# Performance work log

Hardware: AMD Instinct MI355X
Metric: run time of the kernel (lower is better)

Reference implementation:

```python
import jax, jax.numpy as jnp
import numpy as np

TOP_K = 2

def setup_inputs() -> dict:
    key = jax.random.key(0)
    k0, k1, k2, k3 = jax.random.split(key, 4)
    B, S, H, I, E = 2, 2048, 1024, 1408, 8
    hidden_states = jax.random.normal(k0, (B, S, H), dtype=jnp.float32)
    router_weight = jax.random.normal(k1, (E, H), dtype=jnp.float32) * 0.02
    gate_up_proj = jax.random.normal(k2, (E, 2 * I, H), dtype=jnp.float32) * 0.02
    down_proj = jax.random.normal(k3, (E, H, I), dtype=jnp.float32) * 0.02
    return {
        "hidden_states": hidden_states,
        "router_weight": router_weight,
        "gate_up_proj": gate_up_proj,
        "down_proj": down_proj,
    }

def reference(hidden_states, router_weight, gate_up_proj, down_proj):
    B, S, H = hidden_states.shape
    E = router_weight.shape[0]
    x = hidden_states.reshape(-1, H)                       # [T, H]
    T = x.shape[0]
    # Router: logits -> float32 softmax -> top-k (matches torch: topk on probs)
    logits = x @ router_weight.T                           # [T, E]
    probs = jax.nn.softmax(logits.astype(jnp.float32), axis=-1)
    topw, topi = jax.lax.top_k(probs, TOP_K)               # [T, K]
    topw = topw.astype(x.dtype)
    # Per-token combine weights over experts (zero for non-selected experts).
    combine = jnp.zeros((T, E), dtype=x.dtype)
    combine = combine.at[jnp.arange(T)[:, None], topi].set(topw)  # [T, E]
    # Dense grouped expert compute (same math as gather-GEMM-scatter loop:
    # tokens not routed to expert e get combine weight 0).
    gu = jnp.einsum('th,eoh->teo', x, gate_up_proj)        # [T, E, 2I]
    g, u = jnp.split(gu, 2, axis=-1)                       # [T, E, I] each
    h = jax.nn.silu(g) * u                                 # [T, E, I]
    y = jnp.einsum('tei,ehi->teh', h, down_proj)           # [T, E, H]
    out = jnp.einsum('teh,te->th', y, combine)             # [T, H]
    return out.reshape(B, S, H)
```

## Files before the change

kernel.cpp:

```cpp
#include <hip/hip_runtime.h>
#include <math.h>

#define NTOK 4096
#define HDIM 1024
#define NEXP 8
#define IDIM 1408
#define TWO_I 2816
#define BM 128
#define BK 32
#define NRB 72
#define ROWCAP (NRB * BM)

typedef _Float16 f16x8 __attribute__((ext_vector_type(8)));
typedef float f32x4 __attribute__((ext_vector_type(4)));

typedef __attribute__((address_space(1))) const unsigned int gu32;
typedef __attribute__((address_space(3))) unsigned int lu32;
__device__ __forceinline__ void async16(const void* g, void* l) {
  __builtin_amdgcn_global_load_lds((gu32*)g, (lu32*)l, 16, 0, 0);
}

__device__ __forceinline__ void seg_prefix(const int* __restrict__ counts, int* aof) {
  int o = 0; aof[0] = 0;
#pragma unroll
  for (int i = 0; i < 8; i++) { o += (counts[i] + 127) & ~127; aof[i + 1] = o; }
}

extern "C" __global__ void moe_init(int* counts, int* cursor, int* tok) {
  int i = blockIdx.x * 256 + threadIdx.x;
  if (i < NEXP) { counts[i] = 0; cursor[i] = 0; }
  if (i < ROWCAP) tok[i] = -1;
}

#define NG8 (NEXP * TWO_I * HDIM / 8)
#define ND8 (NEXP * HDIM * IDIM / 8)
extern "C" __global__ void moe_cvtw(const float* __restrict__ gup, const float* __restrict__ dp,
                                    _Float16* __restrict__ guph, _Float16* __restrict__ dph) {
  int i = blockIdx.x * 256 + threadIdx.x;
  const float4* s; uint4* d; size_t idx;
  if (i < NG8) { s = (const float4*)gup; d = (uint4*)guph; idx = i; }
  else if (i < NG8 + ND8) { s = (const float4*)dp; d = (uint4*)dph; idx = i - NG8; }
  else return;
  float4 a = s[idx * 2], b = s[idx * 2 + 1];
  union { _Float16 h[8]; uint4 u; } p;
  p.h[0] = (_Float16)a.x; p.h[1] = (_Float16)a.y; p.h[2] = (_Float16)a.z; p.h[3] = (_Float16)a.w;
  p.h[4] = (_Float16)b.x; p.h[5] = (_Float16)b.y; p.h[6] = (_Float16)b.z; p.h[7] = (_Float16)b.w;
  d[idx] = p.u;
}

extern "C" __global__ void moe_router(const float* __restrict__ x,
                                      const float* __restrict__ rw,
                                      int* __restrict__ topi,
                                      float* __restrict__ topw,
                                      _Float16* __restrict__ xh) {
  int w = threadIdx.x >> 6, lane = threadIdx.x & 63;
  int t = blockIdx.x * 4 + w;
  const float4* xp = (const float4*)(x + (size_t)t * HDIM);
  const float4* rp = (const float4*)rw;
  float acc[NEXP];
#pragma unroll
  for (int e = 0; e < NEXP; e++) acc[e] = 0.f;
#pragma unroll
  for (int i = 0; i < HDIM / 256; i++) {
    float4 xv = xp[i * 64 + lane];
    union { _Float16 h[4]; uint2 u; } pk;
    pk.h[0] = (_Float16)xv.x; pk.h[1] = (_Float16)xv.y;
    pk.h[2] = (_Float16)xv.z; pk.h[3] = (_Float16)xv.w;
    *(uint2*)(xh + (size_t)t * HDIM + i * 256 + lane * 4) = pk.u;
#pragma unroll
    for (int e = 0; e < NEXP; e++) {
      float4 rv = rp[e * 256 + i * 64 + lane];
      acc[e] += xv.x * rv.x + xv.y * rv.y + xv.z * rv.z + xv.w * rv.w;
    }
  }
#pragma unroll
  for (int e = 0; e < NEXP; e++) {
#pragma unroll
    for (int off = 32; off > 0; off >>= 1) acc[e] += __shfl_down(acc[e], off);
  }
  if (lane == 0) {
    float m = acc[0];
    for (int e = 1; e < NEXP; e++) m = fmaxf(m, acc[e]);
    float p[NEXP], s = 0.f;
    for (int e = 0; e < NEXP; e++) { p[e] = __expf(acc[e] - m); s += p[e]; }
    float inv = 1.f / s;
    int i0 = 0; float b0 = p[0];
    for (int e = 1; e < NEXP; e++) if (p[e] > b0) { b0 = p[e]; i0 = e; }
    int i1 = -1; float b1 = -1.f;
    for (int e = 0; e < NEXP; e++) if (e != i0 && p[e] > b1) { b1 = p[e]; i1 = e; }
    topi[t * 2] = i0; topi[t * 2 + 1] = i1;
    topw[t * 2] = b0 * inv; topw[t * 2 + 1] = b1 * inv;
  }
}

extern "C" __global__ void moe_count(const int* __restrict__ topi, int* __restrict__ counts) {
  __shared__ int cnt[NEXP];
  if (threadIdx.x < NEXP) cnt[threadIdx.x] = 0;
  __syncthreads();
  int t = blockIdx.x * 256 + threadIdx.x;
  atomicAdd(&cnt[topi[t * 2]], 1);
  atomicAdd(&cnt[topi[t * 2 + 1]], 1);
  __syncthreads();
  if (threadIdx.x < NEXP) atomicAdd(&counts[threadIdx.x], cnt[threadIdx.x]);
}

extern "C" __global__ void moe_scatter(const int* __restrict__ topi, const float* __restrict__ topw,
                                       const int* __restrict__ counts, int* __restrict__ cursor,
                                       int* __restrict__ tok, float* __restrict__ wrow,
                                       int* __restrict__ rows) {
  __shared__ int cnt[NEXP];
  __shared__ int base[NEXP];
  int aof[9]; seg_prefix(counts, aof);
  int tid = threadIdx.x;
  if (tid < NEXP) cnt[tid] = 0;
  __syncthreads();
  int t = blockIdx.x * 256 + tid;
  int e0 = topi[t * 2], e1 = topi[t * 2 + 1];
  int r0 = atomicAdd(&cnt[e0], 1);
  int r1 = atomicAdd(&cnt[e1], 1);
  __syncthreads();
  if (tid < NEXP) base[tid] = atomicAdd(&cursor[tid], cnt[tid]);
  __syncthreads();
  int row0 = aof[e0] + base[e0] + r0;
  int row1 = aof[e1] + base[e1] + r1;
  tok[row0] = t; wrow[row0] = topw[t * 2];     rows[t * 2]     = row0;
  tok[row1] = t; wrow[row1] = topw[t * 2 + 1]; rows[t * 2 + 1] = row1;
}

union SM1 {
  struct { _Float16 a[BM * BK]; _Float16 b[BM * BK]; } st;
  _Float16 ubuf[BM * 66];
};

extern "C" __global__ __launch_bounds__(256) void moe_gemm1(
    const _Float16* __restrict__ xh, const _Float16* __restrict__ guph,
    const int* __restrict__ counts, const int* __restrict__ tok,
    _Float16* __restrict__ hbuf) {
  __shared__ __align__(16) SM1 sm;
  int aof[9]; seg_prefix(counts, aof);
  int fid = blockIdx.x;
  int g = fid & 7, t7 = fid >> 3;
  int jl = t7 % 11, u = t7 / 11;
  int r = u % 9, jh = u / 9;
  int j = jh * 11 + jl;
  int rb = g + 8 * r;
  int row0 = rb * BM;
  if (row0 >= aof[8]) return;
  int e = 0;
#pragma unroll
  for (int i = 0; i < 8; i++) if (row0 >= aof[i]) e = i;

  const int tid = threadIdx.x;
  const int lane = tid & 63, w = tid >> 6;
  const int wm = w & 1, wn = w >> 1;
  const int quad = lane >> 4, l15 = lane & 15;

  f32x4 acc[4][4];
#pragma unroll
  for (int im = 0; im < 4; im++)
#pragma unroll
    for (int in = 0; in < 4; in++) acc[im][in] = (f32x4){0.f, 0.f, 0.f, 0.f};

  const int lq = lane >> 2;
  const int ls = lane & 3;
  const int gsl = ls ^ ((lq >> 1) & 3);
  const int rA0 = w * 16 + lq, rA1 = rA0 + 64;
  int tA0 = tok[row0 + rA0]; tA0 = tA0 < 0 ? 0 : tA0;
  int tA1 = tok[row0 + rA1]; tA1 = tA1 < 0 ? 0 : tA1;
  const _Float16* gA0 = xh + (size_t)tA0 * HDIM + gsl * 8;
  const _Float16* gA1 = xh + (size_t)tA1 * HDIM + gsl * 8;
  const _Float16* eb = guph + (size_t)e * TWO_I * HDIM;
  const _Float16* gB0 = eb + (size_t)(j * 64 + rA0) * HDIM + gsl * 8;
  const _Float16* gB1 = eb + (size_t)(IDIM + j * 64 + rA0) * HDIM + gsl * 8;
  _Float16* lA0 = &sm.st.a[w * 512];
  _Float16* lA1 = &sm.st.a[(w + 4) * 512];
  _Float16* lB0 = &sm.st.b[w * 512];
  _Float16* lB1 = &sm.st.b[(w + 4) * 512];

  const int qsw = (quad ^ ((l15 >> 1) & 3)) * 8;

  for (int kb = 0; kb < HDIM / BK; kb++) {
    async16(gA0, lA0); async16(gA1, lA1);
    async16(gB0, lB0); async16(gB1, lB1);
    gA0 += BK; gA1 += BK; gB0 += BK; gB1 += BK;
    __syncthreads();
    f16x8 av[4], bv[4];
#pragma unroll
    for (int im = 0; im < 4; im++)
      av[im] = *(const f16x8*)&sm.st.a[(wm * 64 + im * 16 + l15) * BK + qsw];
#pragma unroll
    for (int in = 0; in < 4; in++)
      bv[in] = *(const f16x8*)&sm.st.b[(wn * 64 + in * 16 + l15) * BK + qsw];
#pragma unroll
    for (int im = 0; im < 4; im++)
#pragma unroll
      for (int in = 0; in < 4; in++)
        acc[im][in] = __builtin_amdgcn_mfma_f32_16x16x32_f16(av[im], bv[in], acc[im][in], 0, 0, 0);
    __syncthreads();
  }

  if (wn == 1) {
#pragma unroll
    for (int im = 0; im < 4; im++)
#pragma unroll
      for (int in = 0; in < 4; in++)
#pragma unroll
        for (int r2 = 0; r2 < 4; r2++)
          sm.ubuf[(wm * 64 + im * 16 + quad * 4 + r2) * 66 + in * 16 + l15] = (_Float16)acc[im][in][r2];
  }
  __syncthreads();
  if (wn == 0) {
#pragma unroll
    for (int im = 0; im < 4; im++)
#pragma unroll
      for (int in = 0; in < 4; in++)
#pragma unroll
        for (int r2 = 0; r2 < 4; r2++) {
          float gg = acc[im][in][r2];
          float uu = (float)sm.ubuf[(wm * 64 + im * 16 + quad * 4 + r2) * 66 + in * 16 + l15];
          float hh = gg / (1.f + __expf(-gg)) * uu;
          int row = row0 + wm * 64 + im * 16 + quad * 4 + r2;
          hbuf[(size_t)row * IDIM + j * 64 + in * 16 + l15] = (_Float16)hh;
        }
  }
}

extern "C" __global__ __launch_bounds__(256) void moe_gemm2(
    const _Float16* __restrict__ hbuf, const _Float16* __restrict__ dph,
    const int* __restrict__ counts, const float* __restrict__ wrow,
    _Float16* __restrict__ yh) {
  __shared__ __align__(16) struct { _Float16 a[BM * BK]; _Float16 b[BM * BK]; } sm;
  int aof[9]; seg_prefix(counts, aof);
  int fid = blockIdx.x;
  int g = fid & 7, t7 = fid >> 3;
  int cb = t7 & 7, r = t7 >> 3;
  int rb = g + 8 * r;
  int row0 = rb * BM;
  if (row0 >= aof[8]) return;
  int e = 0;
#pragma unroll
  for (int i = 0; i < 8; i++) if (row0 >= aof[i]) e = i;

  const int tid = threadIdx.x;
  const int lane = tid & 63, w = tid >> 6;
  const int wm = w & 1, wn = w >> 1;
  const int quad = lane >> 4, l15 = lane & 15;

  f32x4 acc[4][4];
#pragma unroll
  for (int im = 0; im < 4; im++)
#pragma unroll
    for (int in = 0; in < 4; in++) acc[im][in] = (f32x4){0.f, 0.f, 0.f, 0.f};

  const int lq = lane >> 2, ls = lane & 3;
  const int gsl = ls ^ ((lq >> 1) & 3);
  const int rA0 = w * 16 + lq;
  const _Float16* gA0 = hbuf + (size_t)(row0 + rA0) * IDIM + gsl * 8;
  const _Float16* gA1 = gA0 + (size_t)64 * IDIM;
  const _Float16* eb = dph + (size_t)e * HDIM * IDIM;
  const _Float16* gB0 = eb + (size_t)(cb * 128 + rA0) * IDIM + gsl * 8;
  const _Float16* gB1 = gB0 + (size_t)64 * IDIM;
  _Float16* lA0 = &sm.a[w * 512];
  _Float16* lA1 = &sm.a[(w + 4) * 512];
  _Float16* lB0 = &sm.b[w * 512];
  _Float16* lB1 = &sm.b[(w + 4) * 512];

  const int qsw = (quad ^ ((l15 >> 1) & 3)) * 8;

  for (int kb = 0; kb < IDIM / BK; kb++) {
    async16(gA0, lA0); async16(gA1, lA1);
    async16(gB0, lB0); async16(gB1, lB1);
    gA0 += BK; gA1 += BK; gB0 += BK; gB1 += BK;
    __syncthreads();
    f16x8 av[4], bv[4];
#pragma unroll
    for (int im = 0; im < 4; im++)
      av[im] = *(const f16x8*)&sm.a[(wm * 64 + im * 16 + l15) * BK + qsw];
#pragma unroll
    for (int in = 0; in < 4; in++)
      bv[in] = *(const f16x8*)&sm.b[(wn * 64 + in * 16 + l15) * BK + qsw];
#pragma unroll
    for (int im = 0; im < 4; im++)
#pragma unroll
      for (int in = 0; in < 4; in++)
        acc[im][in] = __builtin_amdgcn_mfma_f32_16x16x32_f16(av[im], bv[in], acc[im][in], 0, 0, 0);
    __syncthreads();
  }

#pragma unroll
  for (int im = 0; im < 4; im++) {
#pragma unroll
    for (int r2 = 0; r2 < 4; r2++) {
      int row = row0 + wm * 64 + im * 16 + quad * 4 + r2;
      float wgt = wrow[row];
#pragma unroll
      for (int in = 0; in < 4; in++) {
        int col = cb * 128 + wn * 64 + in * 16 + l15;
        yh[(size_t)row * HDIM + col] = (_Float16)(acc[im][in][r2] * wgt);
      }
    }
  }
}

extern "C" __global__ void moe_combine(const _Float16* __restrict__ yh,
                                       const int* __restrict__ rows,
                                       float* __restrict__ out) {
  int i = blockIdx.x * 256 + threadIdx.x;
  int t = i >> 7, c8 = i & 127;
  int rA = rows[t * 2], rB = rows[t * 2 + 1];
  union { uint4 u; _Float16 h[8]; } pa, pb;
  pa.u = ((const uint4*)(yh + (size_t)rA * HDIM))[c8];
  pb.u = ((const uint4*)(yh + (size_t)rB * HDIM))[c8];
  float4 o0, o1;
  o0.x = (float)pa.h[0] + (float)pb.h[0]; o0.y = (float)pa.h[1] + (float)pb.h[1];
  o0.z = (float)pa.h[2] + (float)pb.h[2]; o0.w = (float)pa.h[3] + (float)pb.h[3];
  o1.x = (float)pa.h[4] + (float)pb.h[4]; o1.y = (float)pa.h[5] + (float)pb.h[5];
  o1.z = (float)pa.h[6] + (float)pb.h[6]; o1.w = (float)pa.h[7] + (float)pb.h[7];
  ((float4*)out)[(size_t)i * 2] = o0;
  ((float4*)out)[(size_t)i * 2 + 1] = o1;
}

extern "C" void kernel_launch(void* const* d_in, const int* in_sizes, int n_in,
                              void* d_out, int out_size, void* d_ws, size_t ws_size,
                              hipStream_t stream) {
  const float* x   = (const float*)d_in[0];
  const float* rw  = (const float*)d_in[1];
  const float* gup = (const float*)d_in[2];
  const float* dp  = (const float*)d_in[3];
  float* out = (float*)d_out;

  char* ws = (char*)d_ws;
  int*   counts = (int*)ws;
  int*   cursor = (int*)(ws + 64);
  int*   topi   = (int*)(ws + 4096);
  float* topw   = (float*)(ws + 36864);
  int*   tok    = (int*)(ws + 69632);
  float* wrow   = (float*)(ws + 106496);
  int*   rows   = (int*)(ws + 143360);
  _Float16* xh   = (_Float16*)(ws + 176128);
  _Float16* guph = (_Float16*)(ws + 8564736);
  _Float16* dph  = (_Float16*)(ws + 54702080);
  _Float16* hbuf = (_Float16*)(ws + 77770752);
  _Float16* yh   = (_Float16*)(ws + 103723008);

  moe_init<<<(ROWCAP + 255) / 256, 256, 0, stream>>>(counts, cursor, tok);
  moe_router<<<NTOK / 4, 256, 0, stream>>>(x, rw, topi, topw, xh);
  moe_count<<<NTOK / 256, 256, 0, stream>>>(topi, counts);
  moe_scatter<<<NTOK / 256, 256, 0, stream>>>(topi, topw, counts, cursor, tok, wrow, rows);
  moe_cvtw<<<(NG8 + ND8 + 255) / 256, 256, 0, stream>>>(gup, dp, guph, dph);
  moe_gemm1<<<8 * 22 * 9, 256, 0, stream>>>(xh, guph, counts, tok, hbuf);
  moe_gemm2<<<8 * 8 * 9, 256, 0, stream>>>(hbuf, dph, counts, wrow, yh);
  moe_combine<<<NTOK * HDIM / 8 / 256, 256, 0, stream>>>(yh, rows, out);
}
```

Measured before the change: 339.2 us.

## Double K-tile per barrier and remap row blocks contiguously per XCD group

Both GEMM kernels now load a 64-wide K slab as two 32-wide LDS halves per iteration, which halves the number of barrier pairs and keeps more loads in flight. The block-to-row-block mapping is also reworked so that each of the 8 block groups (fid & 7) gets a contiguous range of real row blocks sized from the actual row count. Empty blocks exit early instead of striding past the end, which aims to balance work and improve L2 locality of expert weights. LDS use doubles, which could reduce occupancy. The remap also relies on the grid launching enough blocks per group.

```diff
diff --git a/kernel.cpp b/kernel.cpp
--- a/kernel.cpp
+++ b/kernel.cpp
@@ -7,7 +7,6 @@
 #define IDIM 1408
 #define TWO_I 2816
 #define BM 128
-#define BK 32
 #define NRB 72
 #define ROWCAP (NRB * BM)
 
@@ -128,7 +127,7 @@
 }
 
 union SM1 {
-  struct { _Float16 a[BM * BK]; _Float16 b[BM * BK]; } st;
+  struct { _Float16 a[2][BM * 32]; _Float16 b[2][BM * 32]; } st;
   _Float16 ubuf[BM * 66];
 };
 
@@ -138,14 +137,16 @@
     _Float16* __restrict__ hbuf) {
   __shared__ __align__(16) SM1 sm;
   int aof[9]; seg_prefix(counts, aof);
+  int nl = aof[8] >> 7;
   int fid = blockIdx.x;
-  int g = fid & 7, t7 = fid >> 3;
-  int jl = t7 % 11, u = t7 / 11;
-  int r = u % 9, jh = u / 9;
+  int g = fid & 7, s = fid >> 3;
+  int rb0 = (g * nl) >> 3, ng = (((g + 1) * nl) >> 3) - rb0;
+  if (s >= ng * 22) return;
+  int jl = s % 11, u = s / 11;
+  int r = u % ng, jh = u / ng;
   int j = jh * 11 + jl;
-  int rb = g + 8 * r;
+  int rb = rb0 + r;
   int row0 = rb * BM;
-  if (row0 >= aof[8]) return;
   int e = 0;
 #pragma unroll
   for (int i = 0; i < 8; i++) if (row0 >= aof[i]) e = i;
@@ -172,30 +173,35 @@
   const _Float16* eb = guph + (size_t)e * TWO_I * HDIM;
   const _Float16* gB0 = eb + (size_t)(j * 64 + rA0) * HDIM + gsl * 8;
   const _Float16* gB1 = eb + (size_t)(IDIM + j * 64 + rA0) * HDIM + gsl * 8;
-  _Float16* lA0 = &sm.st.a[w * 512];
-  _Float16* lA1 = &sm.st.a[(w + 4) * 512];
-  _Float16* lB0 = &sm.st.b[w * 512];
-  _Float16* lB1 = &sm.st.b[(w + 4) * 512];
+  _Float16* lA0k0 = &sm.st.a[0][w * 512];        _Float16* lA0k1 = &sm.st.a[1][w * 512];
+  _Float16* lA1k0 = &sm.st.a[0][(w + 4) * 512];  _Float16* lA1k1 = &sm.st.a[1][(w + 4) * 512];
+  _Float16* lB0k0 = &sm.st.b[0][w * 512];        _Float16* lB0k1 = &sm.st.b[1][w * 512];
+  _Float16* lB1k0 = &sm.st.b[0][(w + 4) * 512];  _Float16* lB1k1 = &sm.st.b[1][(w + 4) * 512];
 
   const int qsw = (quad ^ ((l15 >> 1) & 3)) * 8;
 
-  for (int kb = 0; kb < HDIM / BK; kb++) {
-    async16(gA0, lA0); async16(gA1, lA1);
-    async16(gB0, lB0); async16(gB1, lB1);
-    gA0 += BK; gA1 += BK; gB0 += BK; gB1 += BK;
+  for (int kb = 0; kb < HDIM / 64; kb++) {
+    async16(gA0, lA0k0); async16(gA0 + 32, lA0k1);
+    async16(gA1, lA1k0); async16(gA1 + 32, lA1k1);
+    async16(gB0, lB0k0); async16(gB0 + 32, lB0k1);
+    async16(gB1, lB1k0); async16(gB1 + 32, lB1k1);
+    gA0 += 64; gA1 += 64; gB0 += 64; gB1 += 64;
     __syncthreads();
-    f16x8 av[4], bv[4];
-#pragma unroll
-    for (int im = 0; im < 4; im++)
-      av[im] = *(const f16x8*)&sm.st.a[(wm * 64 + im * 16 + l15) * BK + qsw];
-#pragma unroll
-    for (int in = 0; in < 4; in++)
-      bv[in] = *(const f16x8*)&sm.st.b[(wn * 64 + in * 16 + l15) * BK + qsw];
-#pragma unroll
-    for (int im = 0; im < 4; im++)
+#pragma unroll
+    for (int kh = 0; kh < 2; kh++) {
+      f16x8 av[4], bv[4];
+#pragma unroll
+      for (int im = 0; im < 4; im++)
+        av[im] = *(const f16x8*)&sm.st.a[kh][(wm * 64 + im * 16 + l15) * 32 + qsw];
 #pragma unroll
       for (int in = 0; in < 4; in++)
-        acc[im][in] = __builtin_amdgcn_mfma_f32_16x16x32_f16(av[im], bv[in], acc[im][in], 0, 0, 0);
+        bv[in] = *(const f16x8*)&sm.st.b[kh][(wn * 64 + in * 16 + l15) * 32 + qsw];
+#pragma unroll
+      for (int im = 0; im < 4; im++)
+#pragma unroll
+        for (int in = 0; in < 4; in++)
+          acc[im][in] = __builtin_amdgcn_mfma_f32_16x16x32_f16(av[im], bv[in], acc[im][in], 0, 0, 0);
+    }
     __syncthreads();
   }
 
@@ -229,14 +235,16 @@
     const _Float16* __restrict__ hbuf, const _Float16* __restrict__ dph,
     const int* __restrict__ counts, const float* __restrict__ wrow,
     _Float16* __restrict__ yh) {
-  __shared__ __align__(16) struct { _Float16 a[BM * BK]; _Float16 b[BM * BK]; } sm;
+  __shared__ __align__(16) struct { _Float16 a[2][BM * 32]; _Float16 b[2][BM * 32]; } sm;
   int aof[9]; seg_prefix(counts, aof);
+  int nl = aof[8] >> 7;
   int fid = blockIdx.x;
-  int g = fid & 7, t7 = fid >> 3;
-  int cb = t7 & 7, r = t7 >> 3;
-  int rb = g + 8 * r;
+  int g = fid & 7, s = fid >> 3;
+  int rb0 = (g * nl) >> 3, ng = (((g + 1) * nl) >> 3) - rb0;
+  if (s >= ng * 8) return;
+  int cb = s & 7, r = s >> 3;
+  int rb = rb0 + r;
   int row0 = rb * BM;
-  if (row0 >= aof[8]) return;
   int e = 0;
 #pragma unroll
   for (int i = 0; i < 8; i++) if (row0 >= aof[i]) e = i;
@@ -260,30 +268,35 @@
   const _Float16* eb = dph + (size_t)e * HDIM * IDIM;
   const _Float16* gB0 = eb + (size_t)(cb * 128 + rA0) * IDIM + gsl * 8;
   const _Float16* gB1 = gB0 + (size_t)64 * IDIM;
-  _Float16* lA0 = &sm.a[w * 512];
-  _Float16* lA1 = &sm.a[(w + 4) * 512];
-  _Float16* lB0 = &sm.b[w * 512];
-  _Float16* lB1 = &sm.b[(w + 4) * 512];
+  _Float16* lA0k0 = &sm.a[0][w * 512];        _Float16* lA0k1 = &sm.a[1][w * 512];
+  _Float16* lA1k0 = &sm.a[0][(w + 4) * 512];  _Float16* lA1k1 = &sm.a[1][(w + 4) * 512];
+  _Float16* lB0k0 = &sm.b[0][w * 512];        _Float16* lB0k1 = &sm.b[1][w * 512];
+  _Float16* lB1k0 = &sm.b[0][(w + 4) * 512];  _Float16* lB1k1 = &sm.b[1][(w + 4) * 512];
 
   const int qsw = (quad ^ ((l15 >> 1) & 3)) * 8;
 
-  for (int kb = 0; kb < IDIM / BK; kb++) {
-    async16(gA0, lA0); async16(gA1, lA1);
-    async16(gB0, lB0); async16(gB1, lB1);
-    gA0 += BK; gA1 += BK; gB0 += BK; gB1 += BK;
+  for (int kb = 0; kb < IDIM / 64; kb++) {
+    async16(gA0, lA0k0); async16(gA0 + 32, lA0k1);
+    async16(gA1, lA1k0); async16(gA1 + 32, lA1k1);
+    async16(gB0, lB0k0); async16(gB0 + 32, lB0k1);
+    async16(gB1, lB1k0); async16(gB1 + 32, lB1k1);
+    gA0 += 64; gA1 += 64; gB0 += 64; gB1 += 64;
     __syncthreads();
-    f16x8 av[4], bv[4];
-#pragma unroll
-    for (int im = 0; im < 4; im++)
-      av[im] = *(const f16x8*)&sm.a[(wm * 64 + im * 16 + l15) * BK + qsw];
-#pragma unroll
-    for (int in = 0; in < 4; in++)
-      bv[in] = *(const f16x8*)&sm.b[(wn * 64 + in * 16 + l15) * BK + qsw];
-#pragma unroll
-    for (int im = 0; im < 4; im++)
+#pragma unroll
+    for (int kh = 0; kh < 2; kh++) {
+      f16x8 av[4], bv[4];
+#pragma unroll
+      for (int im = 0; im < 4; im++)
+        av[im] = *(const f16x8*)&sm.a[kh][(wm * 64 + im * 16 + l15) * 32 + qsw];
 #pragma unroll
       for (int in = 0; in < 4; in++)
-        acc[im][in] = __builtin_amdgcn_mfma_f32_16x16x32_f16(av[im], bv[in], acc[im][in], 0, 0, 0);
+        bv[in] = *(const f16x8*)&sm.b[kh][(wn * 64 + in * 16 + l15) * 32 + qsw];
+#pragma unroll
+      for (int im = 0; im < 4; im++)
+#pragma unroll
+        for (int in = 0; in < 4; in++)
+          acc[im][in] = __builtin_amdgcn_mfma_f32_16x16x32_f16(av[im], bv[in], acc[im][in], 0, 0, 0);
+    }
     __syncthreads();
   }
 
```

Result: no change. 341.4 us (+0.7%).
